# Kernel tuning notes

Hardware: AMD Instinct MI355X
Metric: run time of the kernel (lower is better)

Reference implementation:

```python
import jax, jax.numpy as jnp
import numpy as np

N_ANCH = 100800   # 3 * (160^2 + 80^2 + 40^2), YOLOv5 @ 1280
NUM_CLS = 80
IMG_HW = 1280
MAX_DETS = 300    # fixed padding for jit-compatible NMS output
OUT = 224
SCORE_THRESH = 0.1
IOU_THRESH = 0.45
ALLOWED = jnp.array([1, 2, 3, 4, 6, 8, 17, 18, 44], dtype=jnp.int32)
MEAN = jnp.array([0.485, 0.456, 0.406], dtype=jnp.float32).reshape(1, 3, 1, 1)
STD = jnp.array([0.229, 0.224, 0.225], dtype=jnp.float32).reshape(1, 3, 1, 1)


def setup_inputs() -> dict:
    key = jax.random.key(0)
    k1, k2, k3, k4, k5 = jax.random.split(key, 5)
    # realistic YOLO-style raw predictions: cx,cy in-image, modest w,h, gaussian class logits
    cxcy = jax.random.uniform(k1, (1, 2, N_ANCH), dtype=jnp.float32) * IMG_HW
    wh = jax.random.uniform(k2, (1, 2, N_ANCH), dtype=jnp.float32) * 256.0 + 8.0
    obj = jax.random.uniform(k3, (1, 1, N_ANCH), dtype=jnp.float32)
    logits = jax.random.normal(k4, (1, NUM_CLS, N_ANCH), dtype=jnp.float32)
    raw_pred = jnp.concatenate([cxcy, wh, obj, logits], axis=1)  # [1, 5+C, N]
    image = jax.random.uniform(k5, (1, 3, IMG_HW, IMG_HW), dtype=jnp.float32)
    return {"raw_pred": raw_pred, "image": image}


def _pairwise_iou(b):
    # b: [K,4] xyxy
    area = (b[:, 2] - b[:, 0]) * (b[:, 3] - b[:, 1])
    lt = jnp.maximum(b[:, None, :2], b[None, :, :2])
    rb = jnp.minimum(b[:, None, 2:], b[None, :, 2:])
    wh = jnp.clip(rb - lt, 0.0)
    inter = wh[..., 0] * wh[..., 1]
    union = area[:, None] + area[None, :] - inter
    return inter / jnp.maximum(union, 1e-9)


def _nms_keep(iou, valid):
    # greedy NMS over score-sorted boxes; returns boolean keep mask [K]
    K = iou.shape[0]
    idx = jnp.arange(K)

    def body(i, keep):
        suppress = keep[i] & (iou[i] > IOU_THRESH) & (idx > i)
        return keep & ~suppress

    return jax.lax.fori_loop(0, K, body, valid)


def _roi_align(image_chw, boxes):
    # torchvision roi_align, aligned=True, one sample per bin at the bin center
    # (sampling_ratio fixed to 1; see notes). image_chw: [3,H,W], boxes: [M,4]
    C, H, W = image_chw.shape
    grid = (jnp.arange(OUT, dtype=jnp.float32) + 0.5) / OUT  # fractional bin centers

    def one(box):
        x1, y1, x2, y2 = box
        xs = x1 - 0.5 + grid * (x2 - x1)  # [OUT], aligned=True half-pixel offset
        ys = y1 - 0.5 + grid * (y2 - y1)
        vx = (xs >= -1.0) & (xs <= W)
        vy = (ys >= -1.0) & (ys <= H)
        xc = jnp.clip(xs, 0.0, W - 1)
        yc = jnp.clip(ys, 0.0, H - 1)
        x0 = jnp.floor(xc).astype(jnp.int32)
        y0 = jnp.floor(yc).astype(jnp.int32)
        x1i = jnp.minimum(x0 + 1, W - 1)
        y1i = jnp.minimum(y0 + 1, H - 1)
        lx = xc - x0
        ly = yc - y0
        # bilinear gather: [3, OUT, OUT]
        v00 = image_chw[:, y0[:, None], x0[None, :]]
        v01 = image_chw[:, y0[:, None], x1i[None, :]]
        v10 = image_chw[:, y1i[:, None], x0[None, :]]
        v11 = image_chw[:, y1i[:, None], x1i[None, :]]
        top = v00 * (1.0 - lx) + v01 * lx
        bot = v10 * (1.0 - lx) + v11 * lx
        val = top * (1.0 - ly)[None, :, None] + bot * ly[None, :, None]
        return jnp.where(vy[None, :, None] & vx[None, None, :], val, 0.0)

    return jax.vmap(one)(boxes)


def _forward(raw_pred, image):
    x = raw_pred[0].T  # [N, 5+C]
    cx, cy, w, h = x[:, 0], x[:, 1], x[:, 2], x[:, 3]
    boxes = jnp.stack([cx - w / 2, cy - h / 2, cx + w / 2, cy + h / 2], axis=1)
    cls_logits = x[:, 5:]
    scores = cls_logits.max(axis=1)
    classes = cls_logits.argmax(axis=1).astype(jnp.int32) + 1
    # score + allowed-class filter (mask form)
    mask = (scores > SCORE_THRESH) & jnp.isin(classes, ALLOWED)
    masked_scores = jnp.where(mask, scores, jnp.finfo(scores.dtype).min)
    top_scores, top_idx = jax.lax.top_k(masked_scores, MAX_DETS)  # sorted desc
    top_boxes = boxes[top_idx]
    top_classes = classes[top_idx]
    valid = mask[top_idx]
    # greedy NMS over padded top-K candidates
    keep = _nms_keep(_pairwise_iou(top_boxes), valid)
    final_boxes = jnp.where(keep[:, None], top_boxes, 0.0)
    final_scores = jnp.where(keep, top_scores, 0.0)
    final_classes = jnp.where(keep, top_classes, 0)
    # crops: full image first, then RoIAlign crops, normalized once
    full_crop = jax.image.resize(image, (1, 3, OUT, OUT), method='linear', antialias=False)
    roi_crops = _roi_align(image[0], final_boxes)  # [K,3,224,224]
    roi_crops = jnp.where(keep[:, None, None, None], roi_crops, 0.0)
    all_crops = jnp.concatenate([full_crop, roi_crops], axis=0)  # [K+1,3,224,224]
    all_crops = (all_crops - MEAN) / STD
    return final_boxes, final_scores, final_classes, all_crops, keep


def reference(raw_pred, image):
    return _forward(raw_pred, image)
```

## Files before the change

### kernel.cpp

```cpp
#include <hip/hip_runtime.h>
#include <stdint.h>

#define N_ANCH   100800
#define NUM_CLS  80
#define IMG_HW   1280
#define MAX_DETS 300
#define OUTSZ    224
#define CAND_CAP 4096

#define OFF_BOXES   0
#define OFF_SCORES  1200
#define OFF_CLASSES 1500
#define OFF_CROPS   1800
#define CROPS_ELEMS (301 * 3 * 224 * 224)
#define OFF_KEEP    (OFF_CROPS + CROPS_ELEMS)

#define SC_HIST   0
#define SC_KEYS   294976
#define SC_CLS    698176

typedef float f32x4 __attribute__((ext_vector_type(4)));

__device__ __forceinline__ uint32_t fkey(float f) {
    uint32_t u = __float_as_uint(f);
    return (u & 0x80000000u) ? ~u : (u | 0x80000000u);
}
__device__ __forceinline__ float unfkey(uint32_t k) {
    uint32_t u = (k & 0x80000000u) ? (k & 0x7fffffffu) : ~k;
    return __uint_as_float(u);
}

__global__ void k_score(const float* __restrict__ rp, uint32_t* __restrict__ keys,
                        uint32_t* __restrict__ hist, uint32_t* __restrict__ clsarr) {
    int gid = blockIdx.x * 256 + threadIdx.x;
    int grp = gid >> 3;
    int cp  = gid & 7;
    if (grp >= N_ANCH / 4) return;
    int a4 = grp * 4;

    float best[4] = {-3.402823466e38f, -3.402823466e38f, -3.402823466e38f, -3.402823466e38f};
    int   bc[4]   = {0, 0, 0, 0};
    #pragma unroll
    for (int k = 0; k < 10; ++k) {
        int c = cp + 8 * k;
        float4 v = *(const float4*)&rp[(size_t)(5 + c) * N_ANCH + a4];
        if (v.x > best[0]) { best[0] = v.x; bc[0] = c; }
        if (v.y > best[1]) { best[1] = v.y; bc[1] = c; }
        if (v.z > best[2]) { best[2] = v.z; bc[2] = c; }
        if (v.w > best[3]) { best[3] = v.w; bc[3] = c; }
    }
    #pragma unroll
    for (int m = 1; m < 8; m <<= 1) {
        #pragma unroll
        for (int j = 0; j < 4; ++j) {
            float ob = __shfl_xor(best[j], m);
            int   oc = __shfl_xor(bc[j], m);
            if (ob > best[j] || (ob == best[j] && oc < bc[j])) { best[j] = ob; bc[j] = oc; }
        }
    }
    if (cp != 0) return;

    const unsigned long long AM =
        (1ULL << 1) | (1ULL << 2) | (1ULL << 3) | (1ULL << 4) | (1ULL << 6) |
        (1ULL << 8) | (1ULL << 17) | (1ULL << 18) | (1ULL << 44);
    uint32_t kv[4], cv[4];
    #pragma unroll
    for (int k = 0; k < 4; ++k) {
        int cls = bc[k] + 1;
        cv[k] = (uint32_t)cls;
        bool mk = (best[k] > 0.1f) && (cls < 64) && ((AM >> cls) & 1ULL);
        kv[k] = mk ? fkey(best[k]) : 0u;
    }
    *(uint4*)&keys[a4]   = make_uint4(kv[0], kv[1], kv[2], kv[3]);
    *(uint4*)&clsarr[a4] = make_uint4(cv[0], cv[1], cv[2], cv[3]);
    #pragma unroll
    for (int k = 0; k < 4; ++k)
        if (kv[k]) atomicAdd(&hist[kv[k] >> 16], 1u);
}

__global__ void __launch_bounds__(1024) k_detect(const float* __restrict__ rp,
                                                 const uint32_t* __restrict__ clsarr,
                                                 const uint32_t* __restrict__ keys,
                                                 const uint32_t* __restrict__ hist,
                                                 float* __restrict__ out) {
    __shared__ uint32_t ssum[1024];
    __shared__ uint32_t swave[16];
    __shared__ int      sh_ssel;
    __shared__ uint32_t sh_acc;
    __shared__ uint32_t sbin[64];
    __shared__ uint32_t sh_thr;
    __shared__ uint32_t s_cnt;
    __shared__ unsigned long long sb[CAND_CAP];
    __shared__ unsigned long long top[MAX_DETS];
    __shared__ float sbx[MAX_DETS][4];
    __shared__ float sscore[MAX_DETS];
    __shared__ int   scls[MAX_DETS];
    __shared__ __align__(8) uint32_t sup[MAX_DETS][10];
    __shared__ __align__(8) uint32_t kw[10];
    __shared__ __align__(8) uint32_t rnz[10];
    int t = threadIdx.x;

    const uint4* h4 = (const uint4*)(hist + t * 64);
    uint32_t s = 0;
    #pragma unroll
    for (int i = 0; i < 16; ++i) { uint4 v = h4[i]; s += v.x + v.y + v.z + v.w; }
    ssum[t] = s;
    uint32_t ws = s;
    #pragma unroll
    for (int m = 32; m; m >>= 1) ws += __shfl_xor(ws, m);
    if ((t & 63) == 0) swave[t >> 6] = ws;
    if (t == 0) s_cnt = 0;
    __syncthreads();
    if (t == 0) {
        uint32_t acc = 0; int wsel = -1;
        for (int w = 15; w >= 0; --w) {
            uint32_t v = swave[w];
            if (acc + v >= (uint32_t)MAX_DETS) { wsel = w; break; }
            acc += v;
        }
        int ssel = -1;
        if (wsel >= 0) {
            for (int sg = wsel * 64 + 63; sg >= wsel * 64; --sg) {
                uint32_t v = ssum[sg];
                if (acc + v >= (uint32_t)MAX_DETS) { ssel = sg; break; }
                acc += v;
            }
        }
        sh_ssel = ssel; sh_acc = acc;
        if (ssel < 0) sh_thr = 0u;
    }
    __syncthreads();
    int ssel = sh_ssel;
    if (ssel >= 0) {
        if (t < 64) sbin[t] = hist[ssel * 64 + t];
        __syncthreads();
        if (t == 0) {
            uint32_t acc = sh_acc;
            uint32_t bin = 0;
            for (int b = 63; b >= 0; --b) {
                acc += sbin[b];
                if (acc >= (uint32_t)MAX_DETS) { bin = (uint32_t)(ssel * 64 + b); break; }
            }
            sh_thr = bin;
        }
    }
    __syncthreads();

    uint32_t thr = sh_thr;
    for (int i4 = t * 4; i4 < N_ANCH; i4 += 4096) {
        uint4 kv = *(const uint4*)&keys[i4];
        uint32_t ks[4] = {kv.x, kv.y, kv.z, kv.w};
        #pragma unroll
        for (int k = 0; k < 4; ++k) {
            uint32_t key = ks[k];
            if (key != 0u && (key >> 16) >= thr) {
                uint32_t pos = atomicAdd(&s_cnt, 1u);
                if (pos < CAND_CAP) {
                    uint32_t a = (uint32_t)(i4 + k);
                    sb[pos] = ((unsigned long long)key << 32) | (uint32_t)(~a);
                }
            }
        }
    }
    __syncthreads();
    int n = min((int)s_cnt, CAND_CAP);

    if (t < MAX_DETS) top[t] = 0ull;
    for (int i = t; i < MAX_DETS * 10; i += 1024) ((uint32_t*)sup)[i] = 0u;
    if (t < 10) { kw[t] = 0u; rnz[t] = 0u; }
    __syncthreads();

    for (int i = t; i < n; i += 1024) {
        unsigned long long key = sb[i];
        int rank = 0;
        for (int j = 0; j < n; ++j) rank += (sb[j] > key) ? 1 : 0;
        if (rank < MAX_DETS) top[rank] = key;
    }
    __syncthreads();

    if (t < MAX_DETS) {
        unsigned long long key = top[t];
        bool valid = (key != 0ull);
        float score = 0.f; int cls = 0;
        float b0 = 0.f, b1 = 0.f, b2 = 0.f, b3 = 0.f;
        if (valid) {
            uint32_t a = ~(uint32_t)(key & 0xffffffffull);
            score = unfkey((uint32_t)(key >> 32));
            float cx = rp[a], cy = rp[N_ANCH + a];
            float w = rp[2 * N_ANCH + a], h = rp[3 * N_ANCH + a];
            b0 = cx - w * 0.5f; b1 = cy - h * 0.5f;
            b2 = cx + w * 0.5f; b3 = cy + h * 0.5f;
            cls = (int)clsarr[a];
            atomicOr(&kw[t >> 5], 1u << (t & 31));
        }
        sbx[t][0] = b0; sbx[t][1] = b1; sbx[t][2] = b2; sbx[t][3] = b3;
        sscore[t] = score; scls[t] = cls;
    }
    __syncthreads();

    for (int p = t; p < MAX_DETS * MAX_DETS; p += 1024) {
        int i = p / MAX_DETS, j = p % MAX_DETS;
        if (j > i) {
            float ax1 = sbx[i][0], ay1 = sbx[i][1], ax2 = sbx[i][2], ay2 = sbx[i][3];
            float bx1 = sbx[j][0], by1 = sbx[j][1], bx2 = sbx[j][2], by2 = sbx[j][3];
            float areaA = (ax2 - ax1) * (ay2 - ay1);
            float areaB = (bx2 - bx1) * (by2 - by1);
            float ltx = fmaxf(ax1, bx1), lty = fmaxf(ay1, by1);
            float rbx = fminf(ax2, bx2), rby = fminf(ay2, by2);
            float iw = fmaxf(rbx - ltx, 0.f), ih = fmaxf(rby - lty, 0.f);
            float inter = iw * ih;
            float uni = areaA + areaB - inter;
            float iou = inter / fmaxf(uni, 1e-9f);
            if (iou > 0.45f) {
                atomicOr(&sup[i][j >> 5], 1u << (j & 31));
                atomicOr(&rnz[i >> 5], 1u << (i & 31));
            }
        }
    }
    __syncthreads();

    if (t == 0) {
        unsigned long long kwr[5], rnzr[5];
        const unsigned long long* kq = (const unsigned long long*)kw;
        const unsigned long long* rq = (const unsigned long long*)rnz;
        #pragma unroll
        for (int w = 0; w < 5; ++w) { kwr[w] = kq[w]; rnzr[w] = rq[w]; }
        #pragma unroll
        for (int sblk = 0; sblk < 5; ++sblk) {
            int lim = (sblk == 4) ? (MAX_DETS - 4 * 64) : 64;
            for (int i2 = 0; i2 < lim; ++i2) {
                if (((kwr[sblk] >> i2) & 1ull) && ((rnzr[sblk] >> i2) & 1ull)) {
                    int i = sblk * 64 + i2;
                    const unsigned long long* row = (const unsigned long long*)&sup[i][0];
                    unsigned long long r0 = row[0], r1 = row[1], r2 = row[2],
                                       r3 = row[3], r4 = row[4];
                    kwr[0] &= ~r0; kwr[1] &= ~r1; kwr[2] &= ~r2;
                    kwr[3] &= ~r3; kwr[4] &= ~r4;
                }
            }
        }
        unsigned long long* kqo = (unsigned long long*)kw;
        #pragma unroll
        for (int w = 0; w < 5; ++w) kqo[w] = kwr[w];
    }
    __syncthreads();

    if (t < MAX_DETS) {
        bool kp = (kw[t >> 5] >> (t & 31)) & 1u;
        out[OFF_BOXES + t * 4 + 0] = kp ? sbx[t][0] : 0.f;
        out[OFF_BOXES + t * 4 + 1] = kp ? sbx[t][1] : 0.f;
        out[OFF_BOXES + t * 4 + 2] = kp ? sbx[t][2] : 0.f;
        out[OFF_BOXES + t * 4 + 3] = kp ? sbx[t][3] : 0.f;
        out[OFF_SCORES + t]  = kp ? sscore[t] : 0.f;
        out[OFF_CLASSES + t] = kp ? (float)scls[t] : 0.f;
        out[OFF_KEEP + t]    = kp ? 1.f : 0.f;
    }
}

#define TROWS 10
#define TPITCH 272

__device__ __forceinline__ float bilerp_g(const float* __restrict__ ch, float xc, float yc) {
    int x0 = (int)floorf(xc), y0 = (int)floorf(yc);
    int x1 = min(x0 + 1, IMG_HW - 1), y1 = min(y0 + 1, IMG_HW - 1);
    float lx = xc - (float)x0, ly = yc - (float)y0;
    float v00 = ch[y0 * IMG_HW + x0], v01 = ch[y0 * IMG_HW + x1];
    float v10 = ch[y1 * IMG_HW + x0], v11 = ch[y1 * IMG_HW + x1];
    return (v00 * (1.f - lx) + v01 * lx) * (1.f - ly) +
           (v10 * (1.f - lx) + v11 * lx) * ly;
}

__global__ void k_crops(const float* __restrict__ img, float* __restrict__ out) {
    __shared__ float tile[TROWS * TPITCH];
    int bx = blockIdx.x;
    int nc = blockIdx.y;
    int n = nc / 3, c = nc % 3;
    int t = threadIdx.x;
    int q = bx * 256 + t;
    int oy = q / (OUTSZ / 4);
    int ox0 = (q % (OUTSZ / 4)) * 4;
    const float meanv[3] = {0.485f, 0.456f, 0.406f};
    const float stdv[3]  = {0.229f, 0.224f, 0.225f};
    float mean = meanv[c], rstd = 1.0f / stdv[c];
    const float* ch = img + (size_t)c * (IMG_HW * IMG_HW);
    f32x4 v;
    if (n == 0) {
        float sy = ((float)oy + 0.5f) * (1280.0f / 224.0f) - 0.5f;
        #pragma unroll
        for (int k = 0; k < 4; ++k) {
            float sx = ((float)(ox0 + k) + 0.5f) * (1280.0f / 224.0f) - 0.5f;
            v[k] = (bilerp_g(ch, sx, sy) - mean) * rstd;
        }
    } else {
        float kp = out[OFF_KEEP + (n - 1)];
        if (kp == 0.f) {
            float z = (0.f - mean) * rstd;
            v = (f32x4){z, z, z, z};
        } else {
            float4 bxv = *(const float4*)&out[OFF_BOXES + (n - 1) * 4];
            float x1b = bxv.x, y1b = bxv.y, x2b = bxv.z, y2b = bxv.w;
            float bw = x2b - x1b, bh = y2b - y1b;
            int oy_s = (bx * 256) / 56;
            int oy_e = (bx * 256 + 255) / 56;
            float ys0 = y1b - 0.5f + (((float)oy_s + 0.5f) / 224.0f) * bh;
            float ys1 = y1b - 0.5f + (((float)oy_e + 0.5f) / 224.0f) * bh;
            int iy_min = (int)floorf(fminf(fmaxf(ys0, 0.f), 1279.f));
            int iy_max = min((int)floorf(fminf(fmaxf(ys1, 0.f), 1279.f)) + 1, IMG_HW - 1);
            float xs0 = x1b - 0.5f + (0.5f / 224.0f) * bw;
            float xs1 = x1b - 0.5f + (223.5f / 224.0f) * bw;
            int ix_min = (int)floorf(fminf(fmaxf(xs0, 0.f), 1279.f));
            int ix_max = min((int)floorf(fminf(fmaxf(xs1, 0.f), 1279.f)) + 1, IMG_HW - 1);
            int ix_al = ix_min & ~3;
            int rows = iy_max - iy_min + 1;
            int w4   = (ix_max - ix_al + 4) >> 2;
            int total = rows * w4;
            for (int i = t; i < total; i += 256) {
                int r  = i / w4;
                int cc = i - r * w4;
                int gy = iy_min + r;
                int px = ix_al + cc * 4;
                const float* src = ch + (size_t)gy * IMG_HW + px;
                float4 val;
                if ((px + 3 < IMG_HW) || (gy < IMG_HW - 1) || (c < 2)) {
                    val = *(const float4*)src;
                } else {
                    val.x = src[0];
                    val.y = src[min(1, IMG_HW - 1 - px)];
                    val.z = src[min(2, IMG_HW - 1 - px)];
                    val.w = src[min(3, IMG_HW - 1 - px)];
                }
                *(float4*)&tile[r * TPITCH + cc * 4] = val;
            }
            __syncthreads();
            float gy = ((float)oy + 0.5f) / 224.0f;
            float ys = y1b - 0.5f + gy * bh;
            bool vy = (ys >= -1.0f) && (ys <= 1280.0f);
            float ycl = fminf(fmaxf(ys, 0.f), 1279.f);
            int y0 = (int)floorf(ycl);
            int y1i = min(y0 + 1, IMG_HW - 1);
            float ly = ycl - (float)y0;
            int ry0 = (y0 - iy_min) * TPITCH - ix_al;
            int ry1 = (y1i - iy_min) * TPITCH - ix_al;
            #pragma unroll
            for (int k = 0; k < 4; ++k) {
                float gx = ((float)(ox0 + k) + 0.5f) / 224.0f;
                float xs = x1b - 0.5f + gx * bw;
                bool vx = (xs >= -1.0f) && (xs <= 1280.0f);
                float xcl = fminf(fmaxf(xs, 0.f), 1279.f);
                int x0 = (int)floorf(xcl);
                int x1i = min(x0 + 1, IMG_HW - 1);
                float lx = xcl - (float)x0;
                float v00 = tile[ry0 + x0], v01 = tile[ry0 + x1i];
                float v10 = tile[ry1 + x0], v11 = tile[ry1 + x1i];
                float val = (v00 * (1.f - lx) + v01 * lx) * (1.f - ly) +
                            (v10 * (1.f - lx) + v11 * lx) * ly;
                if (!(vx && vy)) val = 0.f;
                v[k] = (val - mean) * rstd;
            }
        }
    }
    f32x4* dst = (f32x4*)(out + OFF_CROPS + (size_t)nc * (OUTSZ * OUTSZ) + oy * OUTSZ + ox0);
    __builtin_nontemporal_store(v, dst);
}

extern "C" void kernel_launch(void* const* d_in, const int* in_sizes, int n_in,
                              void* d_out, int out_size, void* d_ws, size_t ws_size,
                              hipStream_t stream) {
    (void)in_sizes; (void)n_in; (void)out_size; (void)d_ws; (void)ws_size;
    const float* rp  = (const float*)d_in[0];
    const float* img = (const float*)d_in[1];
    float* out = (float*)d_out;
    char* sbase = (char*)d_out + (size_t)OFF_CROPS * sizeof(float);
    uint32_t* hist = (uint32_t*)(sbase + SC_HIST);
    uint32_t* keys = (uint32_t*)(sbase + SC_KEYS);
    uint32_t* clsa = (uint32_t*)(sbase + SC_CLS);

    hipMemsetAsync(sbase, 0, 262144, stream);
    k_score<<<(N_ANCH / 4 * 8 + 255) / 256, 256, 0, stream>>>(rp, keys, hist, clsa);
    k_detect<<<1, 1024, 0, stream>>>(rp, clsa, keys, hist, out);
    dim3 grid(49, 903);
    k_crops<<<grid, 256, 0, stream>>>(img, out);
}
```

Before: 366.3 us.

## Compact candidates with wave-level prefix scan and widen crop threads to 16 outputs

The score kernel now writes only masked candidates, packing score, anchor and class into one 64-bit key, into a compact list through a wave prefix-sum and a single atomic per wave. This replaces the dense key/class arrays and the global 64K-bin histogram. The detect kernel builds a 16K-bin histogram in shared memory from that list, which removes the large memset and the full scans over all anchors. The crop kernel now gives each thread 16 outputs over 16 rows per block, so each staged image tile is reused more. The integer division in tile loading is replaced by a float reciprocal with a correction step. The risk is that candidates beyond LIST_CAP are dropped if more than 16384 anchors pass the mask.

```diff
diff --git a/kernel.cpp b/kernel.cpp
--- a/kernel.cpp
+++ b/kernel.cpp
@@ -7,6 +7,7 @@
 #define MAX_DETS 300
 #define OUTSZ    224
 #define CAND_CAP 4096
+#define LIST_CAP 16384
 
 #define OFF_BOXES   0
 #define OFF_SCORES  1200
@@ -15,9 +16,8 @@
 #define CROPS_ELEMS (301 * 3 * 224 * 224)
 #define OFF_KEEP    (OFF_CROPS + CROPS_ELEMS)
 
-#define SC_HIST   0
-#define SC_KEYS   294976
-#define SC_CLS    698176
+#define SC_CNT    0
+#define SC_CAND   64
 
 typedef float f32x4 __attribute__((ext_vector_type(4)));
 
@@ -30,13 +30,14 @@
     return __uint_as_float(u);
 }
 
-__global__ void k_score(const float* __restrict__ rp, uint32_t* __restrict__ keys,
-                        uint32_t* __restrict__ hist, uint32_t* __restrict__ clsarr) {
+__global__ void k_score(const float* __restrict__ rp,
+                        unsigned long long* __restrict__ cand,
+                        uint32_t* __restrict__ cnt) {
     int gid = blockIdx.x * 256 + threadIdx.x;
     int grp = gid >> 3;
     int cp  = gid & 7;
-    if (grp >= N_ANCH / 4) return;
-    int a4 = grp * 4;
+    bool in = (grp < N_ANCH / 4);
+    int a4 = in ? grp * 4 : 0;
 
     float best[4] = {-3.402823466e38f, -3.402823466e38f, -3.402823466e38f, -3.402823466e38f};
     int   bc[4]   = {0, 0, 0, 0};
@@ -58,37 +59,50 @@
             if (ob > best[j] || (ob == best[j] && oc < bc[j])) { best[j] = ob; bc[j] = oc; }
         }
     }
-    if (cp != 0) return;
 
     const unsigned long long AM =
         (1ULL << 1) | (1ULL << 2) | (1ULL << 3) | (1ULL << 4) | (1ULL << 6) |
         (1ULL << 8) | (1ULL << 17) | (1ULL << 18) | (1ULL << 44);
-    uint32_t kv[4], cv[4];
+    unsigned long long pk[4];
+    int cnt_loc = 0;
+    bool lead = (cp == 0) && in;
     #pragma unroll
     for (int k = 0; k < 4; ++k) {
         int cls = bc[k] + 1;
-        cv[k] = (uint32_t)cls;
-        bool mk = (best[k] > 0.1f) && (cls < 64) && ((AM >> cls) & 1ULL);
-        kv[k] = mk ? fkey(best[k]) : 0u;
-    }
-    *(uint4*)&keys[a4]   = make_uint4(kv[0], kv[1], kv[2], kv[3]);
-    *(uint4*)&clsarr[a4] = make_uint4(cv[0], cv[1], cv[2], cv[3]);
-    #pragma unroll
-    for (int k = 0; k < 4; ++k)
-        if (kv[k]) atomicAdd(&hist[kv[k] >> 16], 1u);
+        bool mk = lead && (best[k] > 0.1f) && (cls < 64) && ((AM >> cls) & 1ULL);
+        uint32_t low = ((0x1FFFFu ^ (uint32_t)(a4 + k)) << 7) | (uint32_t)cls;
+        pk[k] = mk ? (((unsigned long long)fkey(best[k]) << 32) | low) : 0ull;
+        cnt_loc += mk ? 1 : 0;
+    }
+
+    int inc = cnt_loc;
+    #pragma unroll
+    for (int d = 1; d < 64; d <<= 1) {
+        int vv = __shfl_up(inc, d);
+        if ((threadIdx.x & 63) >= d) inc += vv;
+    }
+    int total = __shfl(inc, 63);
+    uint32_t base = 0u;
+    if (((threadIdx.x & 63) == 63) && total > 0) base = atomicAdd(cnt, (uint32_t)total);
+    base = (uint32_t)__shfl((int)base, 63);
+    uint32_t pos = base + (uint32_t)(inc - cnt_loc);
+    #pragma unroll
+    for (int k = 0; k < 4; ++k) {
+        if (pk[k]) {
+            if (pos < LIST_CAP) cand[pos] = pk[k];
+            ++pos;
+        }
+    }
 }
 
 __global__ void __launch_bounds__(1024) k_detect(const float* __restrict__ rp,
-                                                 const uint32_t* __restrict__ clsarr,
-                                                 const uint32_t* __restrict__ keys,
-                                                 const uint32_t* __restrict__ hist,
+                                                 const unsigned long long* __restrict__ cand,
+                                                 const uint32_t* __restrict__ cnt_p,
                                                  float* __restrict__ out) {
+    __shared__ uint32_t lhist[16384];
     __shared__ uint32_t ssum[1024];
     __shared__ uint32_t swave[16];
-    __shared__ int      sh_ssel;
-    __shared__ uint32_t sh_acc;
-    __shared__ uint32_t sbin[64];
-    __shared__ uint32_t sh_thr;
+    __shared__ int      sh_thr;
     __shared__ uint32_t s_cnt;
     __shared__ unsigned long long sb[CAND_CAP];
     __shared__ unsigned long long top[MAX_DETS];
@@ -99,17 +113,25 @@
     __shared__ __align__(8) uint32_t kw[10];
     __shared__ __align__(8) uint32_t rnz[10];
     int t = threadIdx.x;
-
-    const uint4* h4 = (const uint4*)(hist + t * 64);
-    uint32_t s = 0;
-    #pragma unroll
-    for (int i = 0; i < 16; ++i) { uint4 v = h4[i]; s += v.x + v.y + v.z + v.w; }
+    int nl = min((int)(*cnt_p), LIST_CAP);
+
+    #pragma unroll
+    for (int i = 0; i < 16; ++i) lhist[t + i * 1024] = 0u;
+    if (t == 0) s_cnt = 0u;
+    __syncthreads();
+    for (int i = t; i < nl; i += 1024)
+        atomicAdd(&lhist[(uint32_t)(cand[i] >> 50)], 1u);
+    __syncthreads();
+
+    const uint4* h4 = (const uint4*)(&lhist[t * 16]);
+    uint4 v0 = h4[0], v1 = h4[1], v2 = h4[2], v3 = h4[3];
+    uint32_t s = v0.x + v0.y + v0.z + v0.w + v1.x + v1.y + v1.z + v1.w +
+                 v2.x + v2.y + v2.z + v2.w + v3.x + v3.y + v3.z + v3.w;
     ssum[t] = s;
     uint32_t ws = s;
     #pragma unroll
     for (int m = 32; m; m >>= 1) ws += __shfl_xor(ws, m);
     if ((t & 63) == 0) swave[t >> 6] = ws;
-    if (t == 0) s_cnt = 0;
     __syncthreads();
     if (t == 0) {
         uint32_t acc = 0; int wsel = -1;
@@ -118,48 +140,29 @@
             if (acc + v >= (uint32_t)MAX_DETS) { wsel = w; break; }
             acc += v;
         }
-        int ssel = -1;
+        int thr = 0;
         if (wsel >= 0) {
-            for (int sg = wsel * 64 + 63; sg >= wsel * 64; --sg) {
-                uint32_t v = ssum[sg];
-                if (acc + v >= (uint32_t)MAX_DETS) { ssel = sg; break; }
+            int tsel = -1;
+            for (int tg = wsel * 64 + 63; tg >= wsel * 64; --tg) {
+                uint32_t v = ssum[tg];
+                if (acc + v >= (uint32_t)MAX_DETS) { tsel = tg; break; }
                 acc += v;
             }
-        }
-        sh_ssel = ssel; sh_acc = acc;
-        if (ssel < 0) sh_thr = 0u;
-    }
-    __syncthreads();
-    int ssel = sh_ssel;
-    if (ssel >= 0) {
-        if (t < 64) sbin[t] = hist[ssel * 64 + t];
-        __syncthreads();
-        if (t == 0) {
-            uint32_t acc = sh_acc;
-            uint32_t bin = 0;
-            for (int b = 63; b >= 0; --b) {
-                acc += sbin[b];
-                if (acc >= (uint32_t)MAX_DETS) { bin = (uint32_t)(ssel * 64 + b); break; }
-            }
-            sh_thr = bin;
-        }
-    }
-    __syncthreads();
-
-    uint32_t thr = sh_thr;
-    for (int i4 = t * 4; i4 < N_ANCH; i4 += 4096) {
-        uint4 kv = *(const uint4*)&keys[i4];
-        uint32_t ks[4] = {kv.x, kv.y, kv.z, kv.w};
-        #pragma unroll
-        for (int k = 0; k < 4; ++k) {
-            uint32_t key = ks[k];
-            if (key != 0u && (key >> 16) >= thr) {
-                uint32_t pos = atomicAdd(&s_cnt, 1u);
-                if (pos < CAND_CAP) {
-                    uint32_t a = (uint32_t)(i4 + k);
-                    sb[pos] = ((unsigned long long)key << 32) | (uint32_t)(~a);
-                }
-            }
+            for (int b = tsel * 16 + 15; b >= tsel * 16; --b) {
+                acc += lhist[b];
+                if (acc >= (uint32_t)MAX_DETS) { thr = b; break; }
+            }
+        }
+        sh_thr = thr;
+    }
+    __syncthreads();
+
+    uint32_t thr = (uint32_t)sh_thr;
+    for (int i = t; i < nl; i += 1024) {
+        unsigned long long key = cand[i];
+        if ((uint32_t)(key >> 50) >= thr) {
+            uint32_t pos = atomicAdd(&s_cnt, 1u);
+            if (pos < CAND_CAP) sb[pos] = key;
         }
     }
     __syncthreads();
@@ -184,13 +187,14 @@
         float score = 0.f; int cls = 0;
         float b0 = 0.f, b1 = 0.f, b2 = 0.f, b3 = 0.f;
         if (valid) {
-            uint32_t a = ~(uint32_t)(key & 0xffffffffull);
+            uint32_t low = (uint32_t)key;
+            uint32_t a = 0x1FFFFu ^ ((low >> 7) & 0x1FFFFu);
+            cls = (int)(low & 0x7Fu);
             score = unfkey((uint32_t)(key >> 32));
             float cx = rp[a], cy = rp[N_ANCH + a];
             float w = rp[2 * N_ANCH + a], h = rp[3 * N_ANCH + a];
             b0 = cx - w * 0.5f; b1 = cy - h * 0.5f;
             b2 = cx + w * 0.5f; b3 = cy + h * 0.5f;
-            cls = (int)clsarr[a];
             atomicOr(&kw[t >> 5], 1u << (t & 31));
         }
         sbx[t][0] = b0; sbx[t][1] = b1; sbx[t][2] = b2; sbx[t][3] = b3;
@@ -232,10 +236,8 @@
                 if (((kwr[sblk] >> i2) & 1ull) && ((rnzr[sblk] >> i2) & 1ull)) {
                     int i = sblk * 64 + i2;
                     const unsigned long long* row = (const unsigned long long*)&sup[i][0];
-                    unsigned long long r0 = row[0], r1 = row[1], r2 = row[2],
-                                       r3 = row[3], r4 = row[4];
-                    kwr[0] &= ~r0; kwr[1] &= ~r1; kwr[2] &= ~r2;
-                    kwr[3] &= ~r3; kwr[4] &= ~r4;
+                    kwr[0] &= ~row[0]; kwr[1] &= ~row[1]; kwr[2] &= ~row[2];
+                    kwr[3] &= ~row[3]; kwr[4] &= ~row[4];
                 }
             }
         }
@@ -257,7 +259,8 @@
     }
 }
 
-#define TROWS 10
+#define RPB    16
+#define TROWS  22
 #define TPITCH 272
 
 __device__ __forceinline__ float bilerp_g(const float* __restrict__ ch, float xc, float yc) {
@@ -274,36 +277,40 @@
     __shared__ float tile[TROWS * TPITCH];
     int bx = blockIdx.x;
     int nc = blockIdx.y;
-    int n = nc / 3, c = nc % 3;
+    int n = nc / 3, c = nc - n * 3;
     int t = threadIdx.x;
-    int q = bx * 256 + t;
-    int oy = q / (OUTSZ / 4);
-    int ox0 = (q % (OUTSZ / 4)) * 4;
+    int rl = t / 14;
+    int xs14 = t - rl * 14;
+    bool act = (t < 224);
+    int oy = bx * RPB + rl;
+    int ox0 = xs14 * 16;
     const float meanv[3] = {0.485f, 0.456f, 0.406f};
     const float stdv[3]  = {0.229f, 0.224f, 0.225f};
     float mean = meanv[c], rstd = 1.0f / stdv[c];
     const float* ch = img + (size_t)c * (IMG_HW * IMG_HW);
-    f32x4 v;
+    f32x4 v[4];
+
     if (n == 0) {
-        float sy = ((float)oy + 0.5f) * (1280.0f / 224.0f) - 0.5f;
-        #pragma unroll
-        for (int k = 0; k < 4; ++k) {
-            float sx = ((float)(ox0 + k) + 0.5f) * (1280.0f / 224.0f) - 0.5f;
-            v[k] = (bilerp_g(ch, sx, sy) - mean) * rstd;
+        if (act) {
+            float sy = ((float)oy + 0.5f) * (1280.0f / 224.0f) - 0.5f;
+            #pragma unroll
+            for (int k = 0; k < 16; ++k) {
+                float sx = ((float)(ox0 + k) + 0.5f) * (1280.0f / 224.0f) - 0.5f;
+                v[k >> 2][k & 3] = (bilerp_g(ch, sx, sy) - mean) * rstd;
+            }
         }
     } else {
         float kp = out[OFF_KEEP + (n - 1)];
         if (kp == 0.f) {
             float z = (0.f - mean) * rstd;
-            v = (f32x4){z, z, z, z};
+            #pragma unroll
+            for (int k4 = 0; k4 < 4; ++k4) v[k4] = (f32x4){z, z, z, z};
         } else {
             float4 bxv = *(const float4*)&out[OFF_BOXES + (n - 1) * 4];
             float x1b = bxv.x, y1b = bxv.y, x2b = bxv.z, y2b = bxv.w;
             float bw = x2b - x1b, bh = y2b - y1b;
-            int oy_s = (bx * 256) / 56;
-            int oy_e = (bx * 256 + 255) / 56;
-            float ys0 = y1b - 0.5f + (((float)oy_s + 0.5f) / 224.0f) * bh;
-            float ys1 = y1b - 0.5f + (((float)oy_e + 0.5f) / 224.0f) * bh;
+            float ys0 = y1b - 0.5f + (((float)(bx * RPB) + 0.5f) / 224.0f) * bh;
+            float ys1 = y1b - 0.5f + (((float)(bx * RPB + RPB - 1) + 0.5f) / 224.0f) * bh;
             int iy_min = (int)floorf(fminf(fmaxf(ys0, 0.f), 1279.f));
             int iy_max = min((int)floorf(fminf(fmaxf(ys1, 0.f), 1279.f)) + 1, IMG_HW - 1);
             float xs0 = x1b - 0.5f + (0.5f / 224.0f) * bw;
@@ -314,9 +321,12 @@
             int rows = iy_max - iy_min + 1;
             int w4   = (ix_max - ix_al + 4) >> 2;
             int total = rows * w4;
+            float winv = 1.0f / (float)w4;
             for (int i = t; i < total; i += 256) {
-                int r  = i / w4;
+                int r  = (int)((float)i * winv);
                 int cc = i - r * w4;
+                if (cc < 0)        { r--; cc += w4; }
+                else if (cc >= w4) { r++; cc -= w4; }
                 int gy = iy_min + r;
                 int px = ix_al + cc * 4;
                 const float* src = ch + (size_t)gy * IMG_HW + px;
@@ -332,35 +342,41 @@
                 *(float4*)&tile[r * TPITCH + cc * 4] = val;
             }
             __syncthreads();
-            float gy = ((float)oy + 0.5f) / 224.0f;
-            float ys = y1b - 0.5f + gy * bh;
-            bool vy = (ys >= -1.0f) && (ys <= 1280.0f);
-            float ycl = fminf(fmaxf(ys, 0.f), 1279.f);
-            int y0 = (int)floorf(ycl);
-            int y1i = min(y0 + 1, IMG_HW - 1);
-            float ly = ycl - (float)y0;
-            int ry0 = (y0 - iy_min) * TPITCH - ix_al;
-            int ry1 = (y1i - iy_min) * TPITCH - ix_al;
-            #pragma unroll
-            for (int k = 0; k < 4; ++k) {
-                float gx = ((float)(ox0 + k) + 0.5f) / 224.0f;
-                float xs = x1b - 0.5f + gx * bw;
-                bool vx = (xs >= -1.0f) && (xs <= 1280.0f);
-                float xcl = fminf(fmaxf(xs, 0.f), 1279.f);
-                int x0 = (int)floorf(xcl);
-                int x1i = min(x0 + 1, IMG_HW - 1);
-                float lx = xcl - (float)x0;
-                float v00 = tile[ry0 + x0], v01 = tile[ry0 + x1i];
-                float v10 = tile[ry1 + x0], v11 = tile[ry1 + x1i];
-                float val = (v00 * (1.f - lx) + v01 * lx) * (1.f - ly) +
-                            (v10 * (1.f - lx) + v11 * lx) * ly;
-                if (!(vx && vy)) val = 0.f;
-                v[k] = (val - mean) * rstd;
-            }
-        }
-    }
-    f32x4* dst = (f32x4*)(out + OFF_CROPS + (size_t)nc * (OUTSZ * OUTSZ) + oy * OUTSZ + ox0);
-    __builtin_nontemporal_store(v, dst);
+            if (act) {
+                float gy = ((float)oy + 0.5f) / 224.0f;
+                float ys = y1b - 0.5f + gy * bh;
+                bool vy = (ys >= -1.0f) && (ys <= 1280.0f);
+                float ycl = fminf(fmaxf(ys, 0.f), 1279.f);
+                int y0 = (int)floorf(ycl);
+                int y1i = min(y0 + 1, IMG_HW - 1);
+                float ly = ycl - (float)y0;
+                int ry0 = (y0 - iy_min) * TPITCH - ix_al;
+                int ry1 = (y1i - iy_min) * TPITCH - ix_al;
+                #pragma unroll
+                for (int k = 0; k < 16; ++k) {
+                    float gx = ((float)(ox0 + k) + 0.5f) / 224.0f;
+                    float xs = x1b - 0.5f + gx * bw;
+                    bool vx = (xs >= -1.0f) && (xs <= 1280.0f);
+                    float xcl = fminf(fmaxf(xs, 0.f), 1279.f);
+                    int x0 = (int)floorf(xcl);
+                    int x1i = min(x0 + 1, IMG_HW - 1);
+                    float lx = xcl - (float)x0;
+                    float v00 = tile[ry0 + x0], v01 = tile[ry0 + x1i];
+                    float v10 = tile[ry1 + x0], v11 = tile[ry1 + x1i];
+                    float val = (v00 * (1.f - lx) + v01 * lx) * (1.f - ly) +
+                                (v10 * (1.f - lx) + v11 * lx) * ly;
+                    if (!(vx && vy)) val = 0.f;
+                    v[k >> 2][k & 3] = (val - mean) * rstd;
+                }
+            }
+        }
+    }
+    if (act) {
+        float* dst = out + OFF_CROPS + (size_t)nc * (OUTSZ * OUTSZ) + (size_t)oy * OUTSZ + ox0;
+        #pragma unroll
+        for (int k4 = 0; k4 < 4; ++k4)
+            __builtin_nontemporal_store(v[k4], (f32x4*)(dst + k4 * 4));
+    }
 }
 
 extern "C" void kernel_launch(void* const* d_in, const int* in_sizes, int n_in,
@@ -371,13 +387,12 @@
     const float* img = (const float*)d_in[1];
     float* out = (float*)d_out;
     char* sbase = (char*)d_out + (size_t)OFF_CROPS * sizeof(float);
-    uint32_t* hist = (uint32_t*)(sbase + SC_HIST);
-    uint32_t* keys = (uint32_t*)(sbase + SC_KEYS);
-    uint32_t* clsa = (uint32_t*)(sbase + SC_CLS);
-
-    hipMemsetAsync(sbase, 0, 262144, stream);
-    k_score<<<(N_ANCH / 4 * 8 + 255) / 256, 256, 0, stream>>>(rp, keys, hist, clsa);
-    k_detect<<<1, 1024, 0, stream>>>(rp, clsa, keys, hist, out);
-    dim3 grid(49, 903);
+    uint32_t* cnt = (uint32_t*)(sbase + SC_CNT);
+    unsigned long long* cand = (unsigned long long*)(sbase + SC_CAND);
+
+    hipMemsetAsync(sbase, 0, 64, stream);
+    k_score<<<(N_ANCH / 4 * 8 + 255) / 256, 256, 0, stream>>>(rp, cand, cnt);
+    k_detect<<<1, 1024, 0, stream>>>(rp, cand, cnt, out);
+    dim3 grid(14, 903);
     k_crops<<<grid, 256, 0, stream>>>(img, out);
 }
```

New measurement: 391.6 us. +6.9%, slower.
